# Performance work log

Measured on AMD Instinct MI355X. Metric: run time of the kernel, lower is better.

Reference implementation:

```python
import jax, jax.numpy as jnp
import numpy as np

T, S, B = 512, 512, 8
D, H = 512, 8
HD = D // H
L = 8            # nlabels
F = 2048         # dim_feedforward
EPS = 1e-5


def _ln(x, s, b):
    m = x.mean(-1, keepdims=True)
    v = ((x - m) ** 2).mean(-1, keepdims=True)
    return (x - m) * jax.lax.rsqrt(v + EPS) * s + b


def setup_inputs() -> dict:
    key = jax.random.key(0)
    ks = jax.random.split(key, 20)
    p = lambda i, shape: jax.random.normal(ks[i], shape, jnp.float32) * 0.02
    z = lambda n: jnp.zeros((n,), jnp.float32)
    return {
        "tgt": jax.random.normal(ks[0], (T, B, D), jnp.float32),
        "edge_mask": jax.random.uniform(ks[1], (B, L, T, T), dtype=jnp.float32),
        "tgt_padding_mask": jnp.zeros((B, T, T), jnp.bool_),
        "memory": jax.random.normal(ks[2], (S, B, D), jnp.float32),
        # self-attn (GNN matrix relational attention)
        "sa_q_w": p(3, (D, D)), "sa_q_b": z(D),
        "sa_k_w": p(4, (D, D)), "sa_k_b": z(D),
        "sa_v_w": p(5, (D, D)), "sa_v_b": z(D),
        "sa_rel": p(6, (L, HD, HD)),
        "sa_out_w": p(7, (D, D)), "sa_out_b": z(D),
        # cross-attn (torch MultiheadAttention packed in_proj)
        "ca_in_w": p(8, (3 * D, D)), "ca_in_b": z(3 * D),
        "ca_out_w": p(9, (D, D)), "ca_out_b": z(D),
        # FFN
        "lin1_w": p(10, (F, D)), "lin1_b": z(F),
        "lin2_w": p(11, (D, F)), "lin2_b": z(D),
        # layernorms
        "ln1_s": jnp.ones((D,), jnp.float32), "ln1_b": z(D),
        "ln2_s": jnp.ones((D,), jnp.float32), "ln2_b": z(D),
        "ln3_s": jnp.ones((D,), jnp.float32), "ln3_b": z(D),
    }


def reference(tgt, edge_mask, tgt_padding_mask, memory,
              sa_q_w, sa_q_b, sa_k_w, sa_k_b, sa_v_w, sa_v_b, sa_rel,
              sa_out_w, sa_out_b, ca_in_w, ca_in_b, ca_out_w, ca_out_b,
              lin1_w, lin1_b, lin2_w, lin2_b,
              ln1_s, ln1_b, ln2_s, ln2_b, ln3_s, ln3_b):
    scale = 1.0 / np.sqrt(HD).astype(np.float32)

    # ---- edge-aware relational self-attention (dropout = eval/identity) ----
    x = tgt.transpose(1, 0, 2)                       # (B, T, D)
    def heads(y, n):                                 # (B, n, ., HD)
        return y.reshape(B, -1, H, HD).transpose(0, 2, 1, 3)
    q = heads(x @ sa_q_w.T + sa_q_b, T)
    k = heads(x @ sa_k_w.T + sa_k_b, T)
    v = heads(x @ sa_v_w.T + sa_v_b, T)

    scores = jnp.zeros((B, H, T, T), q.dtype)
    for l in range(L):                               # small fixed label set
        kl = jnp.einsum('bhtd,de->bhte', k, sa_rel[l])
        scores = scores + edge_mask[:, l][:, None] * jnp.einsum('bhid,bhjd->bhij', q, kl)
    scores = scores * scale
    scores = jnp.where(tgt_padding_mask[:, None], -1e9, scores)
    attn = jax.nn.softmax(scores, axis=-1)
    o = jnp.einsum('bhij,bhjd->bhid', attn, v).transpose(0, 2, 1, 3).reshape(B, T, D)
    tgt2 = (o @ sa_out_w.T + sa_out_b).transpose(1, 0, 2)   # (T, B, D)
    x1 = _ln(tgt + tgt2, ln1_s, ln1_b)

    # ---- standard cross-attention over encoder memory ----
    wq, wk, wv = ca_in_w[:D], ca_in_w[D:2 * D], ca_in_w[2 * D:]
    bq, bk, bv = ca_in_b[:D], ca_in_b[D:2 * D], ca_in_b[2 * D:]
    cq = heads((x1 @ wq.T + bq).transpose(1, 0, 2), T)       # (B,H,T,HD)
    ck = heads((memory @ wk.T + bk).transpose(1, 0, 2), S)   # (B,H,S,HD)
    cv = heads((memory @ wv.T + bv).transpose(1, 0, 2), S)
    cs = jnp.einsum('bhtd,bhsd->bhts', cq, ck) * scale
    ca = jax.nn.softmax(cs, axis=-1)
    co = jnp.einsum('bhts,bhsd->bhtd', ca, cv).transpose(0, 2, 1, 3).reshape(B, T, D)
    tgt2 = (co @ ca_out_w.T + ca_out_b).transpose(1, 0, 2)
    x2 = _ln(x1 + tgt2, ln2_s, ln2_b)

    # ---- FFN ----
    ffn = jax.nn.relu(x2 @ lin1_w.T + lin1_b) @ lin2_w.T + lin2_b
    return _ln(x2 + ffn, ln3_s, ln3_b)
```

## Files before the change

kernel.cpp:

```cpp
#include <hip/hip_runtime.h>

#define Tn 512
#define Sn 512
#define Bn 8
#define Dn 512
#define Hn 8
#define HDn 64
#define Ln 8
#define Fn 2048
#define SCALE 0.125f

typedef short short8 __attribute__((ext_vector_type(8)));
typedef float floatx4 __attribute__((ext_vector_type(4)));

__device__ __forceinline__ unsigned short f2b(float f) {
    unsigned int u = __float_as_uint(f);
    u += 0x7FFFu + ((u >> 16) & 1u);
    return (unsigned short)(u >> 16);
}

__global__ __launch_bounds__(256) void to_rows_bf16(const float* __restrict__ in,
                                                    unsigned short* __restrict__ out, int T_) {
    size_t n = (size_t)blockIdx.x * 256 + threadIdx.x;
    size_t total = (size_t)T_ * Bn * Dn;
    if (n >= total) return;
    int d = (int)(n & (Dn - 1));
    size_t rt = n >> 9;
    int t = (int)(rt % T_);
    int b = (int)(rt / T_);
    out[n] = f2b(in[((size_t)t * Bn + b) * Dn + d]);
}

__global__ __launch_bounds__(256) void conv_all(
    const float* __restrict__ qw, const float* __restrict__ kw, const float* __restrict__ vw,
    const float* __restrict__ sow, const float* __restrict__ ciw, const float* __restrict__ cow,
    const float* __restrict__ l1w, const float* __restrict__ l2w, const float* __restrict__ rel,
    const float* __restrict__ qbias, const float* __restrict__ kbias, const float* __restrict__ vbias,
    unsigned short* __restrict__ wall, float* __restrict__ bqkv) {
    const int Q = 1 << 18;
    const int total = 16 * Q + Ln * HDn * HDn;
    int i = blockIdx.x * 256 + threadIdx.x;
    if (i < total) {
        int seg = i >> 18, r = i & (Q - 1);
        float v;
        if (seg < 3)       v = (seg == 0 ? qw : (seg == 1 ? kw : vw))[r];
        else if (seg == 3) v = sow[r];
        else if (seg < 7)  v = ciw[(size_t)(seg - 4) * Q + r];
        else if (seg == 7) v = cow[r];
        else if (seg < 12) v = l1w[(size_t)(seg - 8) * Q + r];
        else if (seg < 16) v = l2w[(size_t)(seg - 12) * Q + r];
        else               v = rel[r];
        wall[i] = f2b(v);
    }
    int j = i - total;
    if (j >= 0 && j < 3 * Dn)
        bqkv[j] = (j < Dn ? qbias[j] : (j < 2 * Dn ? kbias[j - Dn] : vbias[j - 2 * Dn]));
}

__device__ __forceinline__ void c_scatter(
    floatx4 v, int gm, int gn, size_t coff, int ldc, float alpha, float bb,
    int mode, int relu, int Tp, void* Cv, void* Cv2, void* Cv3) {
    for (int r = 0; r < 4; ++r) {
        float val = v[r] * alpha + bb;
        if (relu) val = fmaxf(val, 0.0f);
        int m = gm + r;
        if (mode == 0) {
            ((float*)Cv)[coff + (size_t)m * ldc + gn] = val;
        } else if (mode == 1) {
            ((unsigned short*)Cv)[coff + (size_t)m * ldc + gn] = f2b(val);
        } else if (mode == 2) {
            int bq = m / Tp, t = m - bq * Tp;
            ((unsigned short*)Cv)[(((size_t)(bq * Hn + (gn >> 6)) * Tp + t) << 6) + (gn & 63)] = f2b(val);
        } else if (mode == 3) {
            int bq = m / Tp, t = m - bq * Tp;
            ((unsigned short*)Cv)[((size_t)(bq * Hn + (gn >> 6)) * 64 + (gn & 63)) * Tp + t] = f2b(val);
        } else if (mode == 4) {
            int sel = gn >> 9, g2 = gn & 511;
            int bq = m / Tp, t = m - bq * Tp;
            int hh = g2 >> 6, dd = g2 & 63;
            if (sel == 0)
                ((unsigned short*)Cv)[(((size_t)(bq * Hn + hh) * Tp + t) << 6) + dd] = f2b(val);
            else if (sel == 1)
                ((unsigned short*)Cv2)[(((size_t)(bq * Hn + hh) * Tp + t) << 6) + dd] = f2b(val);
            else
                ((unsigned short*)Cv3)[((size_t)(bq * Hn + hh) * 64 + dd) * Tp + t] = f2b(val);
        } else {
            int sel = gn >> 9, g2 = gn & 511;
            int bq = m / Tp, t = m - bq * Tp;
            int hh = g2 >> 6, dd = g2 & 63;
            if (sel == 0)
                ((unsigned short*)Cv)[(((size_t)(bq * Hn + hh) * Tp + t) << 6) + dd] = f2b(val);
            else
                ((unsigned short*)Cv2)[((size_t)(bq * Hn + hh) * 64 + dd) * Tp + t] = f2b(val);
        }
    }
}

__global__ __launch_bounds__(256) void gemm_bf16(
    const unsigned short* __restrict__ A, const unsigned short* __restrict__ W,
    const float* __restrict__ bias, void* __restrict__ Cv, void* __restrict__ Cv2,
    void* __restrict__ Cv3,
    int M, int N, int K, int lda, int ldw, int ldc,
    long sA1, long sA2, long sW1, long sW2, long sC1, long sC2, int zdiv,
    float alpha, int mode, int relu, int Tp) {
    int z = blockIdx.z;
    int z1 = z / zdiv, z2 = z - z1 * zdiv;
    const unsigned short* Ab = A + (size_t)z1 * sA1 + (size_t)z2 * sA2;
    const unsigned short* Wb = W + (size_t)z1 * sW1 + (size_t)z2 * sW2;
    size_t coff = (size_t)z1 * sC1 + (size_t)z2 * sC2;
    int tid = threadIdx.x;
    int lane = tid & 63, wave = tid >> 6;
    int wm = wave & 1, wn = wave >> 1;
    int l16 = lane & 15, quad = lane >> 4;
    int m0 = blockIdx.y * 64 + wm * 32;
    int n0 = blockIdx.x * 64 + wn * 32;

    floatx4 acc00 = {0,0,0,0}, acc01 = {0,0,0,0}, acc10 = {0,0,0,0}, acc11 = {0,0,0,0};
    const unsigned short* a0p = Ab + (size_t)(m0 + l16) * lda + quad * 8;
    const unsigned short* a1p = a0p + (size_t)16 * lda;
    const unsigned short* b0p = Wb + (size_t)(n0 + l16) * ldw + quad * 8;
    const unsigned short* b1p = b0p + (size_t)16 * ldw;

#pragma unroll 2
    for (int kk = 0; kk < K; kk += 32) {
        short8 a0 = *(const short8*)(a0p + kk);
        short8 a1 = *(const short8*)(a1p + kk);
        short8 b0 = *(const short8*)(b0p + kk);
        short8 b1 = *(const short8*)(b1p + kk);
        acc00 = __builtin_amdgcn_mfma_f32_16x16x32_bf16(a0, b0, acc00, 0, 0, 0);
        acc01 = __builtin_amdgcn_mfma_f32_16x16x32_bf16(a0, b1, acc01, 0, 0, 0);
        acc10 = __builtin_amdgcn_mfma_f32_16x16x32_bf16(a1, b0, acc10, 0, 0, 0);
        acc11 = __builtin_amdgcn_mfma_f32_16x16x32_bf16(a1, b1, acc11, 0, 0, 0);
    }
    floatx4 accs[2][2] = {{acc00, acc01}, {acc10, acc11}};
    for (int mt = 0; mt < 2; ++mt)
        for (int nt = 0; nt < 2; ++nt) {
            int gn = n0 + nt * 16 + l16;
            float bb = bias ? bias[gn] : 0.0f;
            c_scatter(accs[mt][nt], m0 + mt * 16 + quad * 4, gn, coff, ldc,
                      alpha, bb, mode, relu, Tp, Cv, Cv2, Cv3);
        }
}

template <int MT, int NT>
__global__ __launch_bounds__(256) void gemmT_bf16(
    const unsigned short* __restrict__ A, const unsigned short* __restrict__ W,
    const float* __restrict__ bias, void* __restrict__ Cv, void* __restrict__ Cv2,
    void* __restrict__ Cv3,
    int K, int lda, int ldw, int ldc,
    float alpha, int mode, int relu, int Tp) {
    int tid = threadIdx.x;
    int lane = tid & 63, wave = tid >> 6;
    int wm = wave & 1, wn = wave >> 1;
    int l16 = lane & 15, quad = lane >> 4;
    int m0 = blockIdx.y * (MT * 32) + wm * (MT * 16);
    int n0 = blockIdx.x * (NT * 32) + wn * (NT * 16);

    floatx4 acc[MT][NT] = {};
    const unsigned short* ap = A + (size_t)(m0 + l16) * lda + quad * 8;
    const unsigned short* bp = W + (size_t)(n0 + l16) * ldw + quad * 8;

    for (int kk = 0; kk < K; kk += 32) {
        short8 a[MT], b[NT];
#pragma unroll
        for (int mt = 0; mt < MT; ++mt)
            a[mt] = *(const short8*)(ap + (size_t)mt * 16 * lda + kk);
#pragma unroll
        for (int nt = 0; nt < NT; ++nt)
            b[nt] = *(const short8*)(bp + (size_t)nt * 16 * ldw + kk);
#pragma unroll
        for (int mt = 0; mt < MT; ++mt)
#pragma unroll
            for (int nt = 0; nt < NT; ++nt)
                acc[mt][nt] = __builtin_amdgcn_mfma_f32_16x16x32_bf16(a[mt], b[nt], acc[mt][nt], 0, 0, 0);
    }
    for (int mt = 0; mt < MT; ++mt)
        for (int nt = 0; nt < NT; ++nt) {
            int gn = n0 + nt * 16 + l16;
            float bb = bias ? bias[gn] : 0.0f;
            c_scatter(acc[mt][nt], m0 + mt * 16 + quad * 4, gn, 0, ldc,
                      alpha, bb, mode, relu, Tp, Cv, Cv2, Cv3);
        }
}

__global__ __launch_bounds__(512, 2) void relsoft_em(
    const unsigned short* __restrict__ uR,
    const unsigned short* __restrict__ kB,
    const float* __restrict__ em,
    const unsigned char* __restrict__ pad,
    unsigned short* __restrict__ P) {
    int b = blockIdx.x >> 5, it = blockIdx.x & 31;
    int tid = threadIdx.x;
    int wave = tid >> 6, lane = tid & 63;
    int l16 = lane & 15, quad = lane >> 4;
    int i = it * 16 + l16;

    __shared__ float emS[2 * 8192];
    __shared__ float redm[2][8][16];
    __shared__ float reds[2][8][16];

    auto stage = [&](int step) {
        int l = step & 7, buf = step & 1;
        const float* rowb = em + (((size_t)b * Ln + l) * Tn + (size_t)it * 16) * Tn;
#pragma unroll
        for (int k = 0; k < 4; ++k) {
            int s = k * 512 + wave * 64 + lane;
            int is = s >> 7, gs = s & 127;
            int colg = (gs & 120) | ((gs & 7) ^ (is & 7));
            const float* gp = rowb + (size_t)is * Tn + colg * 4;
            __builtin_amdgcn_global_load_lds(
                (const __attribute__((address_space(1))) void*)gp,
                (__attribute__((address_space(3))) void*)(emS + (size_t)buf * 8192 +
                                                         (size_t)(k * 512 + wave * 64) * 4),
                16, 0, 0);
        }
    };

    unsigned int puf[4];
#pragma unroll
    for (int jc = 0; jc < 4; ++jc)
        puf[jc] = *(const unsigned int*)(pad + ((size_t)b * Tn + i) * Tn +
                                         wave * 64 + jc * 16 + quad * 4);

    stage(0);

#pragma clang loop unroll(disable)
    for (int hp = 0; hp < 4; ++hp) {
        int h0 = hp * 2;
        short8 kf[2][4][2];
#pragma unroll
        for (int hh = 0; hh < 2; ++hh)
#pragma unroll
            for (int jc = 0; jc < 4; ++jc) {
                const unsigned short* kp = kB + (((size_t)(b * Hn + h0 + hh) * Tn) +
                                                wave * 64 + jc * 16 + l16) * HDn + quad * 8;
                kf[hh][jc][0] = *(const short8*)(kp);
                kf[hh][jc][1] = *(const short8*)(kp + 32);
            }
        floatx4 sacc[2][4] = {};

#pragma clang loop unroll(disable)
        for (int l = 0; l < Ln; ++l) {
            int step = hp * 8 + l;
            int buf = l & 1;
            asm volatile("s_waitcnt vmcnt(0)");
            __builtin_amdgcn_sched_barrier(0);
            __syncthreads();
            if (step + 1 < 32) stage(step + 1);

            const float* rb = emS + (size_t)buf * 8192;
            floatx4 emr[4];
#pragma unroll
            for (int jc = 0; jc < 4; ++jc) {
                int gg = wave * 16 + jc * 4 + quad;
                int gsw = (gg & 120) | ((gg & 7) ^ (l16 & 7));
                emr[jc] = *(const floatx4*)(rb + (size_t)(l16 * 128 + gsw) * 4);
            }
            const unsigned short* up = uR + ((((size_t)(b * Hn + h0) * Ln + l) * Tn) + i) * HDn + quad * 8;
            short8 u0a = *(const short8*)(up);
            short8 u0b = *(const short8*)(up + 32);
            short8 u1a = *(const short8*)(up + (size_t)Ln * Tn * HDn);
            short8 u1b = *(const short8*)(up + (size_t)Ln * Tn * HDn + 32);
#pragma unroll
            for (int jc = 0; jc < 4; ++jc) {
                floatx4 g0 = {0, 0, 0, 0};
                g0 = __builtin_amdgcn_mfma_f32_16x16x32_bf16(kf[0][jc][0], u0a, g0, 0, 0, 0);
                g0 = __builtin_amdgcn_mfma_f32_16x16x32_bf16(kf[0][jc][1], u0b, g0, 0, 0, 0);
                sacc[0][jc] += emr[jc] * g0;
                floatx4 g1 = {0, 0, 0, 0};
                g1 = __builtin_amdgcn_mfma_f32_16x16x32_bf16(kf[1][jc][0], u1a, g1, 0, 0, 0);
                g1 = __builtin_amdgcn_mfma_f32_16x16x32_bf16(kf[1][jc][1], u1b, g1, 0, 0, 0);
                sacc[1][jc] += emr[jc] * g1;
            }
        }

#pragma unroll
        for (int hh = 0; hh < 2; ++hh) {
            float mx = -3.0e38f;
#pragma unroll
            for (int jc = 0; jc < 4; ++jc) {
                floatx4 v = sacc[hh][jc] * SCALE;
                unsigned int pu = puf[jc];
                if (pu) {
                    if (pu & 0x000000FFu) v[0] = -1.0e9f;
                    if (pu & 0x0000FF00u) v[1] = -1.0e9f;
                    if (pu & 0x00FF0000u) v[2] = -1.0e9f;
                    if (pu & 0xFF000000u) v[3] = -1.0e9f;
                }
                sacc[hh][jc] = v;
                mx = fmaxf(mx, fmaxf(fmaxf(v[0], v[1]), fmaxf(v[2], v[3])));
            }
            mx = fmaxf(mx, __shfl_xor(mx, 16, 64));
            mx = fmaxf(mx, __shfl_xor(mx, 32, 64));
            if (quad == 0) redm[hh][wave][l16] = mx;
        }
        __syncthreads();
#pragma unroll
        for (int hh = 0; hh < 2; ++hh) {
            float m = redm[hh][0][l16];
#pragma unroll
            for (int w = 1; w < 8; ++w) m = fmaxf(m, redm[hh][w][l16]);
            float sum = 0.0f;
#pragma unroll
            for (int jc = 0; jc < 4; ++jc) {
                floatx4 v = sacc[hh][jc];
                v[0] = __expf(v[0] - m); v[1] = __expf(v[1] - m);
                v[2] = __expf(v[2] - m); v[3] = __expf(v[3] - m);
                sacc[hh][jc] = v;
                sum += v[0] + v[1] + v[2] + v[3];
            }
            sum += __shfl_xor(sum, 16, 64);
            sum += __shfl_xor(sum, 32, 64);
            if (quad == 0) reds[hh][wave][l16] = sum;
        }
        __syncthreads();
#pragma unroll
        for (int hh = 0; hh < 2; ++hh) {
            float sum = 0.0f;
#pragma unroll
            for (int w = 0; w < 8; ++w) sum += reds[hh][w][l16];
            float inv = 1.0f / sum;
            unsigned short* prow = P + ((size_t)(b * Hn + h0 + hh) * Tn + i) * Tn;
#pragma unroll
            for (int jc = 0; jc < 4; ++jc) {
                floatx4 v = sacc[hh][jc];
                ushort4 o;
                o.x = f2b(v[0] * inv); o.y = f2b(v[1] * inv);
                o.z = f2b(v[2] * inv); o.w = f2b(v[3] * inv);
                *(ushort4*)(prow + wave * 64 + jc * 16 + quad * 4) = o;
            }
        }
    }
}

__global__ __launch_bounds__(256) void relsoft_nc(
    const unsigned short* __restrict__ qB,
    const unsigned short* __restrict__ kB,
    unsigned short* __restrict__ P) {
    int id = blockIdx.x;
    int c = id & 7, h = (id >> 3) & 7, g = id >> 6;
    int u = g * 8 + c;
    int b = u >> 5, it = u & 31;
    int bh = b * Hn + h;
    int wave = threadIdx.x >> 6, lane = threadIdx.x & 63;
    int l16 = lane & 15, quad = lane >> 4;
    int i = it * 16 + l16;
    const int JC = Sn / 64;

    __shared__ float redm[4][16];
    __shared__ float reds[4][16];

    const unsigned short* kp0 = kB + (size_t)bh * Sn * HDn + (size_t)l16 * HDn + quad * 8;
    short8 kf[JC][2];
#pragma unroll
    for (int jc = 0; jc < JC; ++jc) {
        const unsigned short* kp = kp0 + (size_t)(wave * JC + jc) * 16 * HDn;
        kf[jc][0] = *(const short8*)(kp);
        kf[jc][1] = *(const short8*)(kp + 32);
    }
    const unsigned short* ub = qB + (size_t)bh * Tn * HDn + (size_t)i * HDn + quad * 8;
    short8 u0 = *(const short8*)(ub);
    short8 u1 = *(const short8*)(ub + 32);

    floatx4 sacc[JC];
    float mx = -3.0e38f;
#pragma unroll
    for (int jc = 0; jc < JC; ++jc) {
        floatx4 gacc = {0, 0, 0, 0};
        gacc = __builtin_amdgcn_mfma_f32_16x16x32_bf16(kf[jc][0], u0, gacc, 0, 0, 0);
        gacc = __builtin_amdgcn_mfma_f32_16x16x32_bf16(kf[jc][1], u1, gacc, 0, 0, 0);
        floatx4 v = gacc * SCALE;
        sacc[jc] = v;
        mx = fmaxf(mx, fmaxf(fmaxf(v[0], v[1]), fmaxf(v[2], v[3])));
    }
    mx = fmaxf(mx, __shfl_xor(mx, 16, 64));
    mx = fmaxf(mx, __shfl_xor(mx, 32, 64));
    if (quad == 0) redm[wave][l16] = mx;
    __syncthreads();
    mx = fmaxf(fmaxf(redm[0][l16], redm[1][l16]), fmaxf(redm[2][l16], redm[3][l16]));

    float sum = 0.0f;
#pragma unroll
    for (int jc = 0; jc < JC; ++jc) {
        floatx4 v = sacc[jc];
        v[0] = __expf(v[0] - mx); v[1] = __expf(v[1] - mx);
        v[2] = __expf(v[2] - mx); v[3] = __expf(v[3] - mx);
        sacc[jc] = v;
        sum += v[0] + v[1] + v[2] + v[3];
    }
    sum += __shfl_xor(sum, 16, 64);
    sum += __shfl_xor(sum, 32, 64);
    if (quad == 0) reds[wave][l16] = sum;
    __syncthreads();
    sum = (reds[0][l16] + reds[1][l16]) + (reds[2][l16] + reds[3][l16]);
    float inv = 1.0f / sum;

    unsigned short* prow = P + (size_t)bh * Tn * Sn + (size_t)i * Sn;
#pragma unroll
    for (int jc = 0; jc < JC; ++jc) {
        int jt = wave * JC + jc;
        floatx4 v = sacc[jc];
        ushort4 o;
        o.x = f2b(v[0] * inv); o.y = f2b(v[1] * inv);
        o.z = f2b(v[2] * inv); o.w = f2b(v[3] * inv);
        *(ushort4*)(prow + jt * 16 + quad * 4) = o;
    }
}

__global__ __launch_bounds__(256) void ln_kernel(
    const float* __restrict__ a, int a_trans, const float* __restrict__ b2,
    const float* __restrict__ s, const float* __restrict__ bb,
    float* __restrict__ outF, int out_trans, unsigned short* __restrict__ outB) {
    int row = blockIdx.x;
    int b = row >> 9, t = row & (Tn - 1);
    int tid = threadIdx.x;
    size_t ia = a_trans ? ((size_t)(t * Bn + b)) * Dn : (size_t)row * Dn;
    size_t ir = (size_t)row * Dn;
    float x0 = a[ia + tid];
    float x1 = a[ia + tid + 256];
    if (b2) { x0 += b2[ir + tid]; x1 += b2[ir + tid + 256]; }
    float s1 = x0 + x1, s2 = x0 * x0 + x1 * x1;
    for (int off = 32; off; off >>= 1) {
        s1 += __shfl_xor(s1, off, 64);
        s2 += __shfl_xor(s2, off, 64);
    }
    __shared__ float red[2][4];
    int wave = tid >> 6, lane = tid & 63;
    if (lane == 0) { red[0][wave] = s1; red[1][wave] = s2; }
    __syncthreads();
    float ts1 = red[0][0] + red[0][1] + red[0][2] + red[0][3];
    float ts2 = red[1][0] + red[1][1] + red[1][2] + red[1][3];
    float mean = ts1 * (1.0f / Dn);
    float var = ts2 * (1.0f / Dn) - mean * mean;
    float rs = rsqrtf(var + 1e-5f);
    float y0 = (x0 - mean) * rs * s[tid] + bb[tid];
    float y1 = (x1 - mean) * rs * s[tid + 256] + bb[tid + 256];
    size_t io = out_trans ? ((size_t)(t * Bn + b)) * Dn : ir;
    if (outF) { outF[io + tid] = y0; outF[io + tid + 256] = y1; }
    if (outB) { outB[ir + tid] = f2b(y0); outB[ir + tid + 256] = f2b(y1); }
}

extern "C" void kernel_launch(void* const* d_in, const int* in_sizes, int n_in,
                              void* d_out, int out_size, void* d_ws, size_t ws_size,
                              hipStream_t stream) {
    const float* tgt      = (const float*)d_in[0];
    const float* em       = (const float*)d_in[1];
    const unsigned char* pad = (const unsigned char*)d_in[2];
    const float* memr     = (const float*)d_in[3];
    const float* sa_q_w   = (const float*)d_in[4];
    const float* sa_q_b   = (const float*)d_in[5];
    const float* sa_k_w   = (const float*)d_in[6];
    const float* sa_k_b   = (const float*)d_in[7];
    const float* sa_v_w   = (const float*)d_in[8];
    const float* sa_v_b   = (const float*)d_in[9];
    const float* sa_rel   = (const float*)d_in[10];
    const float* sa_out_w = (const float*)d_in[11];
    const float* sa_out_b = (const float*)d_in[12];
    const float* ca_in_w  = (const float*)d_in[13];
    const float* ca_in_b  = (const float*)d_in[14];
    const float* ca_out_w = (const float*)d_in[15];
    const float* ca_out_b = (const float*)d_in[16];
    const float* lin1_w   = (const float*)d_in[17];
    const float* lin1_b   = (const float*)d_in[18];
    const float* lin2_w   = (const float*)d_in[19];
    const float* lin2_b   = (const float*)d_in[20];
    const float* ln1_s    = (const float*)d_in[21];
    const float* ln1_b    = (const float*)d_in[22];
    const float* ln2_s    = (const float*)d_in[23];
    const float* ln2_b    = (const float*)d_in[24];
    const float* ln3_s    = (const float*)d_in[25];
    const float* ln3_b    = (const float*)d_in[26];

    const size_t BT = (size_t)Bn * Tn;
    const size_t Q  = 1 << 18;

    char* ws = (char*)d_ws;
    size_t off = 0;
    auto alloc = [&](size_t bytes) -> char* {
        char* p = ws + off;
        off += (bytes + 255) & ~(size_t)255;
        return p;
    };
    unsigned short* xb   = (unsigned short*)alloc(BT * Dn * 2);
    unsigned short* mb   = (unsigned short*)alloc(BT * Dn * 2);
    unsigned short* wall = (unsigned short*)alloc((16 * Q + Ln * HDn * HDn) * 2);
    float*          bqkv = (float*)alloc(3 * Dn * 4);
    unsigned short* qb   = (unsigned short*)alloc(BT * Dn * 2);
    unsigned short* kb   = (unsigned short*)alloc(BT * Dn * 2);
    unsigned short* vtb  = (unsigned short*)alloc(BT * Dn * 2);
    unsigned short* ur   = (unsigned short*)alloc((size_t)Bn * Hn * Ln * Tn * HDn * 2);
    unsigned short* pb   = (unsigned short*)alloc((size_t)Bn * Hn * Tn * Tn * 2);
    unsigned short* ob   = (unsigned short*)alloc(BT * Dn * 2);
    float*          t2f  = (float*)alloc(BT * Dn * 4);
    float*          x1f  = (float*)alloc(BT * Dn * 4);
    unsigned short* x1b  = (unsigned short*)alloc(BT * Dn * 2);
    float*          x2f  = (float*)alloc(BT * Dn * 4);
    unsigned short* x2b  = (unsigned short*)alloc(BT * Dn * 2);
    unsigned short* hid  = (unsigned short*)alloc(BT * Fn * 2);
    (void)ws_size; (void)in_sizes; (void)n_in; (void)out_size;

    unsigned short* wqkv = wall;
    unsigned short* wsao = wall + 3 * Q;
    unsigned short* wcain = wall + 4 * Q;
    unsigned short* wcao = wall + 7 * Q;
    unsigned short* wlin1 = wall + 8 * Q;
    unsigned short* wlin2 = wall + 12 * Q;
    unsigned short* wrel = wall + 16 * Q;

    auto gemm = [&](const unsigned short* A, const unsigned short* W, const float* bias,
                    void* C, void* C2, void* C3, int M, int N, int K, int lda, int ldw, int ldc,
                    long sA1, long sA2, long sW1, long sW2, long sC1, long sC2,
                    int zdiv, int batches, float alpha, int mode, int relu, int Tp) {
        dim3 g(N / 64, M / 64, batches);
        gemm_bf16<<<g, 256, 0, stream>>>(A, W, bias, C, C2, C3, M, N, K, lda, ldw, ldc,
                                         sA1, sA2, sW1, sW2, sC1, sC2, zdiv,
                                         alpha, mode, relu, Tp);
    };
    auto gemmBig = [&](const unsigned short* A, const unsigned short* W, const float* bias,
                       void* C, void* C2, void* C3, int M, int N, int K,
                       int lda, int ldw, int ldc, float alpha, int mode, int relu, int Tp) {
        dim3 g(N / 128, M / 128, 1);
        gemmT_bf16<4, 4><<<g, 256, 0, stream>>>(A, W, bias, C, C2, C3, K, lda, ldw, ldc,
                                                alpha, mode, relu, Tp);
    };
    auto gemmMed = [&](const unsigned short* A, const unsigned short* W, const float* bias,
                       void* C, void* C2, void* C3, int M, int N, int K,
                       int lda, int ldw, int ldc, float alpha, int mode, int relu, int Tp) {
        dim3 g(N / 64, M / 128, 1);
        gemmT_bf16<4, 2><<<g, 256, 0, stream>>>(A, W, bias, C, C2, C3, K, lda, ldw, ldc,
                                                alpha, mode, relu, Tp);
    };

    to_rows_bf16<<<dim3((BT * Dn + 255) / 256), 256, 0, stream>>>(tgt, xb, Tn);
    to_rows_bf16<<<dim3((BT * Dn + 255) / 256), 256, 0, stream>>>(memr, mb, Sn);
    conv_all<<<dim3((16 * Q + Ln * HDn * HDn + 3 * Dn + 255) / 256), 256, 0, stream>>>(
        sa_q_w, sa_k_w, sa_v_w, sa_out_w, ca_in_w, ca_out_w, lin1_w, lin2_w, sa_rel,
        sa_q_b, sa_k_b, sa_v_b, wall, bqkv);

    gemmBig(xb, wqkv, bqkv, qb, kb, vtb, (int)BT, 3 * Dn, Dn, Dn, Dn, 0, 1.0f, 4, 0, Tn);
    gemm(qb, wrel, nullptr, ur, nullptr, nullptr, Tn, HDn, HDn, HDn, HDn, HDn,
         (long)Tn * HDn, 0, 0, (long)HDn * HDn, (long)Ln * Tn * HDn, (long)Tn * HDn,
         Ln, Bn * Hn * Ln, 1.0f, 1, 0, 0);
    relsoft_em<<<dim3(256), 512, 0, stream>>>(ur, kb, em, pad, pb);
    gemm(pb, vtb, nullptr, ob, nullptr, nullptr, Tn, HDn, Tn, Tn, Tn, Dn,
         (long)Hn * Tn * Tn, (long)Tn * Tn, (long)Hn * HDn * Tn, (long)HDn * Tn,
         (long)Tn * Dn, 64, Hn, Bn * Hn, 1.0f, 1, 0, 0);
    gemmMed(ob, wsao, sa_out_b, t2f, nullptr, nullptr, (int)BT, Dn, Dn, Dn, Dn, Dn,
            1.0f, 0, 0, 0);
    ln_kernel<<<dim3((int)BT), 256, 0, stream>>>(tgt, 1, t2f, ln1_s, ln1_b, x1f, 0, x1b);

    gemmMed(x1b, wcain, ca_in_b, qb, nullptr, nullptr, (int)BT, Dn, Dn, Dn, Dn, 0,
            1.0f, 2, 0, Tn);
    gemmBig(mb, wcain + (size_t)Dn * Dn, ca_in_b + Dn, kb, vtb, nullptr, (int)BT, 2 * Dn, Dn,
            Dn, Dn, 0, 1.0f, 5, 0, Sn);
    relsoft_nc<<<dim3(2048), 256, 0, stream>>>(qb, kb, pb);
    gemm(pb, vtb, nullptr, ob, nullptr, nullptr, Tn, HDn, Sn, Sn, Sn, Dn,
         (long)Hn * Tn * Sn, (long)Tn * Sn, (long)Hn * HDn * Sn, (long)HDn * Sn,
         (long)Tn * Dn, 64, Hn, Bn * Hn, 1.0f, 1, 0, 0);
    gemmMed(ob, wcao, ca_out_b, t2f, nullptr, nullptr, (int)BT, Dn, Dn, Dn, Dn, Dn,
            1.0f, 0, 0, 0);
    ln_kernel<<<dim3((int)BT), 256, 0, stream>>>(x1f, 0, t2f, ln2_s, ln2_b, x2f, 0, x2b);

    gemmBig(x2b, wlin1, lin1_b, hid, nullptr, nullptr, (int)BT, Fn, Dn, Dn, Dn, Fn,
            1.0f, 1, 1, 0);
    gemmMed(hid, wlin2, lin2_b, t2f, nullptr, nullptr, (int)BT, Dn, Fn, Fn, Fn, Dn,
            1.0f, 0, 0, 0);
    ln_kernel<<<dim3((int)BT), 256, 0, stream>>>(x2f, 0, t2f, ln3_s, ln3_b, (float*)d_out, 1, nullptr);
}
```

Baseline: 641.7 us.

## Split relational softmax kernel across head pairs with triple-buffered edge-mask staging

```diff
diff --git a/kernel.cpp b/kernel.cpp
--- a/kernel.cpp
+++ b/kernel.cpp
@@ -189,30 +189,35 @@
     const float* __restrict__ em,
     const unsigned char* __restrict__ pad,
     unsigned short* __restrict__ P) {
-    int b = blockIdx.x >> 5, it = blockIdx.x & 31;
+    int id = blockIdx.x;
+    int r5 = id & 31, q5 = id >> 5;
+    int hp = r5 >> 3;
+    int uu = q5 * 8 + (r5 & 7);
+    int b = uu >> 5, it = uu & 31;
+    int h0 = hp * 2;
     int tid = threadIdx.x;
     int wave = tid >> 6, lane = tid & 63;
     int l16 = lane & 15, quad = lane >> 4;
     int i = it * 16 + l16;
 
-    __shared__ float emS[2 * 8192];
+    __shared__ float emS[3 * 8 * 1024];
+    __shared__ float uS[256 * 32];
     __shared__ float redm[2][8][16];
     __shared__ float reds[2][8][16];
 
-    auto stage = [&](int step) {
-        int l = step & 7, buf = step & 1;
-        const float* rowb = em + (((size_t)b * Ln + l) * Tn + (size_t)it * 16) * Tn;
+    const float* emBase = em + ((size_t)b * Ln * Tn + (size_t)it * 16) * Tn;
+
+    auto stageEM = [&](int sl, int buf) {
+        const float* rowb = emBase + (size_t)sl * Tn * Tn;
+        float* wb = emS + (size_t)(buf * 8 + wave) * 1024;
 #pragma unroll
         for (int k = 0; k < 4; ++k) {
-            int s = k * 512 + wave * 64 + lane;
-            int is = s >> 7, gs = s & 127;
-            int colg = (gs & 120) | ((gs & 7) ^ (is & 7));
-            const float* gp = rowb + (size_t)is * Tn + colg * 4;
+            int s = k * 64 + lane;
+            int rr = s >> 4, sc = s & 15;
+            const float* gp = rowb + (size_t)rr * Tn + (wave * 16 + (sc ^ rr)) * 4;
             __builtin_amdgcn_global_load_lds(
                 (const __attribute__((address_space(1))) void*)gp,
-                (__attribute__((address_space(3))) void*)(emS + (size_t)buf * 8192 +
-                                                         (size_t)(k * 512 + wave * 64) * 4),
-                16, 0, 0);
+                (__attribute__((address_space(3))) void*)(wb + k * 256), 16, 0, 0);
         }
     };
 
@@ -221,114 +226,141 @@
     for (int jc = 0; jc < 4; ++jc)
         puf[jc] = *(const unsigned int*)(pad + ((size_t)b * Tn + i) * Tn +
                                          wave * 64 + jc * 16 + quad * 4);
-
-    stage(0);
-
+    short8 kf[2][4][2];
+#pragma unroll
+    for (int hh = 0; hh < 2; ++hh)
+#pragma unroll
+        for (int jc = 0; jc < 4; ++jc) {
+            const unsigned short* kp = kB + ((size_t)(b * Hn + h0 + hh) * Tn +
+                                             wave * 64 + jc * 16 + l16) * HDn + quad * 8;
+            kf[hh][jc][0] = *(const short8*)(kp);
+            kf[hh][jc][1] = *(const short8*)(kp + 32);
+        }
+    __builtin_amdgcn_sched_barrier(0);
+    asm volatile("s_waitcnt vmcnt(0)");
+    __builtin_amdgcn_sched_barrier(0);
+
+#pragma unroll
+    for (int k = 0; k < 4; ++k) {
+        int s = k * 64 + lane;
+        int rl = s >> 3, sc = s & 7;
+        int row = wave * 32 + rl;
+        int hh = row >> 7, rem = row & 127;
+        int ll = rem >> 4, ii = rem & 15;
+        const unsigned short* gp = uR + (((size_t)(b * Hn + h0 + hh) * Ln + ll) * Tn +
+                                         it * 16 + ii) * HDn + (sc ^ (ii & 7)) * 8;
+        __builtin_amdgcn_global_load_lds(
+            (const __attribute__((address_space(1))) void*)gp,
+            (__attribute__((address_space(3))) void*)(uS + (size_t)wave * 1024 + k * 256),
+            16, 0, 0);
+    }
+    __builtin_amdgcn_sched_barrier(0);
+    stageEM(0, 0);
+    __builtin_amdgcn_sched_barrier(0);
+    stageEM(1, 1);
+    __builtin_amdgcn_sched_barrier(0);
+    stageEM(2, 2);
+    __builtin_amdgcn_sched_barrier(0);
+    asm volatile("s_waitcnt vmcnt(12)");
+    __builtin_amdgcn_sched_barrier(0);
+    __builtin_amdgcn_s_barrier();
+
+    floatx4 sacc[2][4] = {};
 #pragma clang loop unroll(disable)
-    for (int hp = 0; hp < 4; ++hp) {
-        int h0 = hp * 2;
-        short8 kf[2][4][2];
-#pragma unroll
-        for (int hh = 0; hh < 2; ++hh)
-#pragma unroll
-            for (int jc = 0; jc < 4; ++jc) {
-                const unsigned short* kp = kB + (((size_t)(b * Hn + h0 + hh) * Tn) +
-                                                wave * 64 + jc * 16 + l16) * HDn + quad * 8;
-                kf[hh][jc][0] = *(const short8*)(kp);
-                kf[hh][jc][1] = *(const short8*)(kp + 32);
+    for (int l = 0; l < Ln; ++l) {
+        int buf = l % 3;
+        if (l < 6)       { asm volatile("s_waitcnt vmcnt(8)"); }
+        else if (l == 6) { asm volatile("s_waitcnt vmcnt(4)"); }
+        else             { asm volatile("s_waitcnt vmcnt(0)"); }
+        __builtin_amdgcn_sched_barrier(0);
+
+        const float* rb = emS + (size_t)(buf * 8 + wave) * 1024;
+        floatx4 emr[4];
+#pragma unroll
+        for (int jc = 0; jc < 4; ++jc) {
+            int sc = (jc * 4 + quad) ^ l16;
+            emr[jc] = *(const floatx4*)(rb + l16 * 64 + sc * 4);
+        }
+        const float* u0row = uS + (size_t)((0 * Ln + l) * 16 + l16) * 32;
+        const float* u1row = uS + (size_t)((1 * Ln + l) * 16 + l16) * 32;
+        int us0 = (quad ^ (l16 & 7)) * 4;
+        int us1 = ((quad + 4) ^ (l16 & 7)) * 4;
+        short8 u0a = *(const short8*)(u0row + us0);
+        short8 u0b = *(const short8*)(u0row + us1);
+        short8 u1a = *(const short8*)(u1row + us0);
+        short8 u1b = *(const short8*)(u1row + us1);
+        asm volatile("s_waitcnt lgkmcnt(0)");
+        __builtin_amdgcn_sched_barrier(0);
+        if (l + 3 < Ln) stageEM(l + 3, buf);
+        __builtin_amdgcn_sched_barrier(0);
+
+#pragma unroll
+        for (int jc = 0; jc < 4; ++jc) {
+            floatx4 g0 = {0, 0, 0, 0};
+            g0 = __builtin_amdgcn_mfma_f32_16x16x32_bf16(kf[0][jc][0], u0a, g0, 0, 0, 0);
+            g0 = __builtin_amdgcn_mfma_f32_16x16x32_bf16(kf[0][jc][1], u0b, g0, 0, 0, 0);
+            sacc[0][jc] += emr[jc] * g0;
+            floatx4 g1 = {0, 0, 0, 0};
+            g1 = __builtin_amdgcn_mfma_f32_16x16x32_bf16(kf[1][jc][0], u1a, g1, 0, 0, 0);
+            g1 = __builtin_amdgcn_mfma_f32_16x16x32_bf16(kf[1][jc][1], u1b, g1, 0, 0, 0);
+            sacc[1][jc] += emr[jc] * g1;
+        }
+    }
+
+#pragma unroll
+    for (int hh = 0; hh < 2; ++hh) {
+        float mx = -3.0e38f;
+#pragma unroll
+        for (int jc = 0; jc < 4; ++jc) {
+            floatx4 v = sacc[hh][jc] * SCALE;
+            unsigned int pu = puf[jc];
+            if (pu) {
+                if (pu & 0x000000FFu) v[0] = -1.0e9f;
+                if (pu & 0x0000FF00u) v[1] = -1.0e9f;
+                if (pu & 0x00FF0000u) v[2] = -1.0e9f;
+                if (pu & 0xFF000000u) v[3] = -1.0e9f;
             }
-        floatx4 sacc[2][4] = {};
-
-#pragma clang loop unroll(disable)
-        for (int l = 0; l < Ln; ++l) {
-            int step = hp * 8 + l;
-            int buf = l & 1;
-            asm volatile("s_waitcnt vmcnt(0)");
-            __builtin_amdgcn_sched_barrier(0);
-            __syncthreads();
-            if (step + 1 < 32) stage(step + 1);
-
-            const float* rb = emS + (size_t)buf * 8192;
-            floatx4 emr[4];
-#pragma unroll
-            for (int jc = 0; jc < 4; ++jc) {
-                int gg = wave * 16 + jc * 4 + quad;
-                int gsw = (gg & 120) | ((gg & 7) ^ (l16 & 7));
-                emr[jc] = *(const floatx4*)(rb + (size_t)(l16 * 128 + gsw) * 4);
-            }
-            const unsigned short* up = uR + ((((size_t)(b * Hn + h0) * Ln + l) * Tn) + i) * HDn + quad * 8;
-            short8 u0a = *(const short8*)(up);
-            short8 u0b = *(const short8*)(up + 32);
-            short8 u1a = *(const short8*)(up + (size_t)Ln * Tn * HDn);
-            short8 u1b = *(const short8*)(up + (size_t)Ln * Tn * HDn + 32);
-#pragma unroll
-            for (int jc = 0; jc < 4; ++jc) {
-                floatx4 g0 = {0, 0, 0, 0};
-                g0 = __builtin_amdgcn_mfma_f32_16x16x32_bf16(kf[0][jc][0], u0a, g0, 0, 0, 0);
-                g0 = __builtin_amdgcn_mfma_f32_16x16x32_bf16(kf[0][jc][1], u0b, g0, 0, 0, 0);
-                sacc[0][jc] += emr[jc] * g0;
-                floatx4 g1 = {0, 0, 0, 0};
-                g1 = __builtin_amdgcn_mfma_f32_16x16x32_bf16(kf[1][jc][0], u1a, g1, 0, 0, 0);
-                g1 = __builtin_amdgcn_mfma_f32_16x16x32_bf16(kf[1][jc][1], u1b, g1, 0, 0, 0);
-                sacc[1][jc] += emr[jc] * g1;
-            }
-        }
-
-#pragma unroll
-        for (int hh = 0; hh < 2; ++hh) {
-            float mx = -3.0e38f;
-#pragma unroll
-            for (int jc = 0; jc < 4; ++jc) {
-                floatx4 v = sacc[hh][jc] * SCALE;
-                unsigned int pu = puf[jc];
-                if (pu) {
-                    if (pu & 0x000000FFu) v[0] = -1.0e9f;
-                    if (pu & 0x0000FF00u) v[1] = -1.0e9f;
-                    if (pu & 0x00FF0000u) v[2] = -1.0e9f;
-                    if (pu & 0xFF000000u) v[3] = -1.0e9f;
-                }
-                sacc[hh][jc] = v;
-                mx = fmaxf(mx, fmaxf(fmaxf(v[0], v[1]), fmaxf(v[2], v[3])));
-            }
-            mx = fmaxf(mx, __shfl_xor(mx, 16, 64));
-            mx = fmaxf(mx, __shfl_xor(mx, 32, 64));
-            if (quad == 0) redm[hh][wave][l16] = mx;
-        }
-        __syncthreads();
-#pragma unroll
-        for (int hh = 0; hh < 2; ++hh) {
-            float m = redm[hh][0][l16];
-#pragma unroll
-            for (int w = 1; w < 8; ++w) m = fmaxf(m, redm[hh][w][l16]);
-            float sum = 0.0f;
-#pragma unroll
-            for (int jc = 0; jc < 4; ++jc) {
-                floatx4 v = sacc[hh][jc];
-                v[0] = __expf(v[0] - m); v[1] = __expf(v[1] - m);
-                v[2] = __expf(v[2] - m); v[3] = __expf(v[3] - m);
-                sacc[hh][jc] = v;
-                sum += v[0] + v[1] + v[2] + v[3];
-            }
-            sum += __shfl_xor(sum, 16, 64);
-            sum += __shfl_xor(sum, 32, 64);
-            if (quad == 0) reds[hh][wave][l16] = sum;
-        }
-        __syncthreads();
-#pragma unroll
-        for (int hh = 0; hh < 2; ++hh) {
-            float sum = 0.0f;
-#pragma unroll
-            for (int w = 0; w < 8; ++w) sum += reds[hh][w][l16];
-            float inv = 1.0f / sum;
-            unsigned short* prow = P + ((size_t)(b * Hn + h0 + hh) * Tn + i) * Tn;
-#pragma unroll
-            for (int jc = 0; jc < 4; ++jc) {
-                floatx4 v = sacc[hh][jc];
-                ushort4 o;
-                o.x = f2b(v[0] * inv); o.y = f2b(v[1] * inv);
-                o.z = f2b(v[2] * inv); o.w = f2b(v[3] * inv);
-                *(ushort4*)(prow + wave * 64 + jc * 16 + quad * 4) = o;
-            }
+            sacc[hh][jc] = v;
+            mx = fmaxf(mx, fmaxf(fmaxf(v[0], v[1]), fmaxf(v[2], v[3])));
+        }
+        mx = fmaxf(mx, __shfl_xor(mx, 16, 64));
+        mx = fmaxf(mx, __shfl_xor(mx, 32, 64));
+        if (quad == 0) redm[hh][wave][l16] = mx;
+    }
+    __syncthreads();
+#pragma unroll
+    for (int hh = 0; hh < 2; ++hh) {
+        float m = redm[hh][0][l16];
+#pragma unroll
+        for (int w = 1; w < 8; ++w) m = fmaxf(m, redm[hh][w][l16]);
+        float sum = 0.0f;
+#pragma unroll
+        for (int jc = 0; jc < 4; ++jc) {
+            floatx4 v = sacc[hh][jc];
+            v[0] = __expf(v[0] - m); v[1] = __expf(v[1] - m);
+            v[2] = __expf(v[2] - m); v[3] = __expf(v[3] - m);
+            sacc[hh][jc] = v;
+            sum += v[0] + v[1] + v[2] + v[3];
+        }
+        sum += __shfl_xor(sum, 16, 64);
+        sum += __shfl_xor(sum, 32, 64);
+        if (quad == 0) reds[hh][wave][l16] = sum;
+    }
+    __syncthreads();
+#pragma unroll
+    for (int hh = 0; hh < 2; ++hh) {
+        float sum = 0.0f;
+#pragma unroll
+        for (int w = 0; w < 8; ++w) sum += reds[hh][w][l16];
+        float inv = 1.0f / sum;
+        unsigned short* prow = P + ((size_t)(b * Hn + h0 + hh) * Tn + i) * Tn;
+#pragma unroll
+        for (int jc = 0; jc < 4; ++jc) {
+            floatx4 v = sacc[hh][jc];
+            ushort4 o;
+            o.x = f2b(v[0] * inv); o.y = f2b(v[1] * inv);
+            o.z = f2b(v[2] * inv); o.w = f2b(v[3] * inv);
+            *(ushort4*)(prow + wave * 64 + jc * 16 + quad * 4) = o;
         }
     }
 }
@@ -541,7 +573,7 @@
     gemm(qb, wrel, nullptr, ur, nullptr, nullptr, Tn, HDn, HDn, HDn, HDn, HDn,
          (long)Tn * HDn, 0, 0, (long)HDn * HDn, (long)Ln * Tn * HDn, (long)Tn * HDn,
          Ln, Bn * Hn * Ln, 1.0f, 1, 0, 0);
-    relsoft_em<<<dim3(256), 512, 0, stream>>>(ur, kb, em, pad, pb);
+    relsoft_em<<<dim3(1024), 512, 0, stream>>>(ur, kb, em, pad, pb);
     gemm(pb, vtb, nullptr, ob, nullptr, nullptr, Tn, HDn, Tn, Tn, Tn, Dn,
          (long)Hn * Tn * Tn, (long)Tn * Tn, (long)Hn * HDn * Tn, (long)HDn * Tn,
          (long)Tn * Dn, 64, Hn, Bn * Hn, 1.0f, 1, 0, 0);
```

New measurement: 615.6 us. -4.1%, faster.
